# Optimization experiments

Hardware: AMD Instinct MI355X
Metric: run time of the kernel (lower is better)

Reference implementation:

```python
import jax, jax.numpy as jnp
import numpy as np

B, N, F, H, D = 2, 2048, 1024, 16, 64


def setup_inputs() -> dict:
    key = jax.random.key(0)
    ks = jax.random.split(key, 5)
    s = 0.02
    return {
        "x": jax.random.normal(ks[0], (B, N, F), jnp.float32),
        "w_qkv": (jax.random.normal(ks[1], (3 * H * D, F), jnp.float32) * s),
        "w_out": (jax.random.normal(ks[2], (F, H * D), jnp.float32) * s),
        "w_hp_pre": (jax.random.normal(ks[3], (H, H), jnp.float32) * (1.0 / H)),
        "b_hp_pre": jnp.zeros((H,), jnp.float32),
        "w_hp_post": (jax.random.normal(ks[4], (H, H), jnp.float32) * (1.0 / H)),
        "b_hp_post": jnp.zeros((H,), jnp.float32),
    }


def reference(x, w_qkv, w_out, w_hp_pre, b_hp_pre, w_hp_post, b_hp_post):
    b, n, f = x.shape
    # qkv projection; rearrange 'b n (h d qkv) -> qkv b h n d' (qkv innermost)
    proj = (x @ w_qkv.T).reshape(b, n, H, D, 3)
    q = jnp.transpose(proj[..., 0], (0, 2, 1, 3))  # b h n d
    k = jnp.transpose(proj[..., 1], (0, 2, 1, 3))
    v = jnp.transpose(proj[..., 2], (0, 2, 1, 3))
    kv = jnp.stack([k, v], axis=0)  # (2, b, h, n, d) -- returned cache

    scale = D ** -0.5
    dots = jnp.einsum('bhid,bhjd->bhij', q, k) * scale
    # pre talking-heads: 1x1 conv over head channel
    dots = jnp.einsum('gh,bhij->bgij', w_hp_pre, dots) + b_hp_pre[None, :, None, None]
    attn = jax.nn.softmax(dots, axis=-1)
    # post talking-heads
    attn = jnp.einsum('gh,bhij->bgij', w_hp_post, attn) + b_hp_post[None, :, None, None]
    out = jnp.einsum('bhij,bhjd->bhid', attn, v)
    out = jnp.transpose(out, (0, 2, 1, 3)).reshape(b, n, H * D)
    out = out @ w_out.T
    return out, kv
```

## Files before the change

### kernel.cpp

```cpp
#include <hip/hip_runtime.h>
#include <hip/hip_bf16.h>
#include <cstdint>
#include <cstddef>

#define B_ 2
#define N_ 2048
#define F_ 1024
#define H_ 16
#define D_ 64

typedef float f32x4 __attribute__((ext_vector_type(4)));
typedef short s16x8 __attribute__((ext_vector_type(8)));
typedef short s16x4 __attribute__((ext_vector_type(4)));

__device__ __forceinline__ unsigned short f2bf(float f) {
  union { __hip_bfloat16 h; unsigned short u; } c;
  c.h = __float2bfloat16(f);
  return c.u;
}

__device__ __forceinline__ void bar_lgkm() {
  asm volatile("s_waitcnt lgkmcnt(0)" ::: "memory");
  __builtin_amdgcn_s_barrier();
}

__global__ __launch_bounds__(256) void cvt_bf16(const float* __restrict__ in,
                                                unsigned short* __restrict__ out,
                                                int n8) {
  const int t = blockIdx.x * 256 + threadIdx.x;
  if (t >= n8) return;
  const float4* p = (const float4*)in + (size_t)t * 2;
  float4 a = p[0], b = p[1];
  s16x8 o;
  o[0] = f2bf(a.x); o[1] = f2bf(a.y); o[2] = f2bf(a.z); o[3] = f2bf(a.w);
  o[4] = f2bf(b.x); o[5] = f2bf(b.y); o[6] = f2bf(b.z); o[7] = f2bf(b.w);
  *((s16x8*)out + t) = o;
}

__global__ __launch_bounds__(256) void cvt_wqkv_perm(const float* __restrict__ in,
                                                     unsigned short* __restrict__ out) {
  const int t = blockIdx.x * 256 + threadIdx.x;
  const int rowp = t >> 7;
  const int kk = (t & 127) * 8;
  const int c = rowp >> 10, rem = rowp & 1023;
  const int h = rem >> 6, d = rem & 63;
  const float* p = in + (size_t)(h * 192 + d * 3 + c) * 1024 + kk;
  float4 a = *(const float4*)p, b = *(const float4*)(p + 4);
  s16x8 o;
  o[0] = f2bf(a.x); o[1] = f2bf(a.y); o[2] = f2bf(a.z); o[3] = f2bf(a.w);
  o[4] = f2bf(b.x); o[5] = f2bf(b.y); o[6] = f2bf(b.z); o[7] = f2bf(b.w);
  *((s16x8*)&out[(size_t)rowp * 1024 + kk]) = o;
}

__global__ __launch_bounds__(256) void cvt_sum4(const float* __restrict__ a,
                                                unsigned short* __restrict__ out) {
  const int t = blockIdx.x * 256 + threadIdx.x;
  const size_t stride = (size_t)B_ * N_ * 1024 / 4;
  float4 x0 = *((const float4*)a + t);
  float4 x1 = *((const float4*)a + stride + t);
  float4 x2 = *((const float4*)a + 2 * stride + t);
  float4 x3 = *((const float4*)a + 3 * stride + t);
  s16x4 o;
  o[0] = f2bf((x0.x + x1.x) + (x2.x + x3.x));
  o[1] = f2bf((x0.y + x1.y) + (x2.y + x3.y));
  o[2] = f2bf((x0.z + x1.z) + (x2.z + x3.z));
  o[3] = f2bf((x0.w + x1.w) + (x2.w + x3.w));
  *((s16x4*)out + t) = o;
}

template <int MODE>
__global__ __launch_bounds__(256) void gemm_bf16(const unsigned short* __restrict__ A,
                                                 const unsigned short* __restrict__ W,
                                                 float* __restrict__ o0,
                                                 unsigned short* __restrict__ oQ,
                                                 unsigned short* __restrict__ oK,
                                                 unsigned short* __restrict__ oVt) {
  __shared__ unsigned short As[128 * 72];
  __shared__ unsigned short Bs[128 * 72];
  const int m0 = blockIdx.y * 128, c0 = blockIdx.x * 128;
  const int tid = threadIdx.x;
  const int wave = tid >> 6, lane = tid & 63;
  const int wm = (wave & 1) * 64, wn = (wave >> 1) * 64;
  const int lm = lane & 15, lq = lane >> 4;
  f32x4 acc[4][4] = {};
  for (int k0 = 0; k0 < 1024; k0 += 64) {
#pragma unroll
    for (int it = 0; it < 4; ++it) {
      const int chunk = it * 256 + tid;
      const int row = chunk >> 3, kq = (chunk & 7) * 8;
      *(float4*)&As[row * 72 + kq] = *(const float4*)&A[(size_t)(m0 + row) * 1024 + k0 + kq];
      *(float4*)&Bs[row * 72 + kq] = *(const float4*)&W[(size_t)(c0 + row) * 1024 + k0 + kq];
    }
    __syncthreads();
#pragma unroll
    for (int ks = 0; ks < 2; ++ks) {
      s16x8 af[4], bfr[4];
#pragma unroll
      for (int i = 0; i < 4; ++i) {
        af[i] = *(const s16x8*)&As[(wm + i * 16 + lm) * 72 + ks * 32 + lq * 8];
        bfr[i] = *(const s16x8*)&Bs[(wn + i * 16 + lm) * 72 + ks * 32 + lq * 8];
      }
#pragma unroll
      for (int i = 0; i < 4; ++i)
#pragma unroll
        for (int j = 0; j < 4; ++j)
          acc[i][j] = __builtin_amdgcn_mfma_f32_16x16x32_bf16(af[i], bfr[j], acc[i][j], 0, 0, 0);
    }
    __syncthreads();
  }
  if (MODE == 1) {
#pragma unroll
    for (int i = 0; i < 4; ++i)
#pragma unroll
      for (int j = 0; j < 4; ++j)
#pragma unroll
        for (int r = 0; r < 4; ++r) {
          const int m = m0 + wm + i * 16 + lq * 4 + r;
          const int col = c0 + wn + j * 16 + lm;
          o0[(size_t)m * 1024 + col] = acc[i][j][r];
        }
  } else {
    const int cls = blockIdx.x >> 3;
    const int colbase = (blockIdx.x & 7) * 128;
    if (cls == 0) {
#pragma unroll
      for (int i = 0; i < 4; ++i)
#pragma unroll
        for (int j = 0; j < 4; ++j) {
          const int cl = colbase + wn + j * 16 + lm;
          const int h = cl >> 6, d = cl & 63;
#pragma unroll
          for (int r = 0; r < 4; ++r) {
            const int m = m0 + wm + i * 16 + lq * 4 + r;
            const int bb = m >> 11, n = m & 2047;
            oQ[(((size_t)bb * H_ + h) * N_ + n) * D_ + d] = f2bf(acc[i][j][r]);
          }
        }
    } else if (cls == 1) {
#pragma unroll
      for (int i = 0; i < 4; ++i)
#pragma unroll
        for (int j = 0; j < 4; ++j) {
          const int cl = colbase + wn + j * 16 + lm;
          const int h = cl >> 6, d = cl & 63;
#pragma unroll
          for (int r = 0; r < 4; ++r) {
            const int m = m0 + wm + i * 16 + lq * 4 + r;
            const int bb = m >> 11, n = m & 2047;
            const size_t idx = (((size_t)bb * H_ + h) * N_ + n) * D_ + d;
            o0[idx] = acc[i][j][r];
            oK[idx] = f2bf(acc[i][j][r]);
          }
        }
    } else {
#pragma unroll
      for (int i = 0; i < 4; ++i) {
        const int n0 = m0 + wm + i * 16 + lq * 4;
        const int bb = n0 >> 11, nl = n0 & 2047;
#pragma unroll
        for (int j = 0; j < 4; ++j) {
          const int cl = colbase + wn + j * 16 + lm;
          const int h = cl >> 6, d = cl & 63;
          s16x4 vp;
#pragma unroll
          for (int r = 0; r < 4; ++r) {
            const size_t idx = (((size_t)bb * H_ + h) * N_ + nl + r) * D_ + d;
            o0[(size_t)B_ * H_ * N_ * D_ + idx] = acc[i][j][r];
            vp[r] = (short)f2bf(acc[i][j][r]);
          }
          *(s16x4*)&oVt[(((size_t)bb * H_ + h) * D_ + d) * N_ + nl] = vp;
        }
      }
    }
  }
}

#define SS_J 20
#define SLOT 320
#define SS_I 644
#define SS_HALF (32 * SS_I + 16)
#define PS_J 36
#define PS_G 1156
#define PS_HALF (16 * PS_G)

__device__ __forceinline__ f32x4 mfma16(s16x8 a, s16x8 b, f32x4 c) {
  return __builtin_amdgcn_mfma_f32_16x16x32_bf16(a, b, c, 0, 0, 0);
}

__device__ __forceinline__ void load_k1(s16x8 (&kr)[2][2],
                                        const unsigned short* __restrict__ Kb,
                                        int b, int h0, int j0, int lm, int lq) {
#pragma unroll
  for (int jt = 0; jt < 2; ++jt) {
    const unsigned short* kp =
        &Kb[(((size_t)(b * H_ + h0) * N_) + j0 + jt * 16 + lm) * D_ + lq * 8];
    kr[jt][0] = *(const s16x8*)kp;
    kr[jt][1] = *(const s16x8*)(kp + 32);
  }
}

__device__ __forceinline__ void load_v1(s16x8 (&vt)[4],
                                        const unsigned short* __restrict__ Vt,
                                        int b, int h0, int j0, int lm, int lq) {
#pragma unroll
  for (int nd = 0; nd < 4; ++nd)
    vt[nd] = *(const s16x8*)&Vt[(((size_t)(b * H_ + h0) * D_) + nd * 16 + lm) * N_ + j0 + lq * 8];
}

__device__ __forceinline__ void scores_phase1(const s16x8 (&aq)[2][2],
                                              const s16x8 (&kr)[2][2],
                                              unsigned short* Sb,
                                              int lm, int lq, int h0) {
#pragma unroll
  for (int jt = 0; jt < 2; ++jt) {
    f32x4 c[2];
    __builtin_amdgcn_s_setprio(1);
#pragma unroll
    for (int mi = 0; mi < 2; ++mi) {
      f32x4 cc = {};
      cc = mfma16(aq[mi][0], kr[jt][0], cc);
      cc = mfma16(aq[mi][1], kr[jt][1], cc);
      c[mi] = cc;
    }
    __builtin_amdgcn_s_setprio(0);
#pragma unroll
    for (int mi = 0; mi < 2; ++mi)
#pragma unroll
      for (int r = 0; r < 4; ++r)
        Sb[(mi * 16 + lq * 4 + r) * SS_I + jt * SLOT + lm * SS_J + h0] = f2bf(c[mi][r]);
  }
}

__global__ __launch_bounds__(1024, 4) void attn_l(const unsigned short* __restrict__ Qb,
                                                  const unsigned short* __restrict__ Kb,
                                                  const float* __restrict__ wpre,
                                                  const float* __restrict__ bpre,
                                                  float* __restrict__ l_glob) {
  __shared__ unsigned short Ssh[SS_HALF];
  const int tid = threadIdx.x;
  const int wave = tid >> 6, lane = tid & 63;
  const int lm = lane & 15, lq = lane >> 4;
  const int b = blockIdx.z, jh = blockIdx.y;
  const int i0 = blockIdx.x * 32;
  const int j00 = jh * 512;
  const int h0 = wave;

  for (int t = tid; t < SS_HALF; t += 1024) Ssh[t] = 0;

  s16x8 aq[2][2];
#pragma unroll
  for (int mi = 0; mi < 2; ++mi)
#pragma unroll
    for (int ks = 0; ks < 2; ++ks)
      aq[mi][ks] = *(const s16x8*)&Qb[(((size_t)(b * H_ + h0) * N_) + i0 + mi * 16 + lm) * D_ + ks * 32 + lq * 8];

  s16x8 apre;
#pragma unroll
  for (int t = 0; t < 8; ++t) apre[t] = 0;
  if (lq < 2)
#pragma unroll
    for (int t = 0; t < 8; ++t) apre[t] = (short)f2bf(wpre[lm * 16 + lq * 8 + t] * 0.125f);
  float bpre_r[4];
#pragma unroll
  for (int r = 0; r < 4; ++r) bpre_r[r] = bpre[lq * 4 + r];

  float lacc[2][4] = {};

  s16x8 kr[2][2];
  load_k1(kr, Kb, b, h0, j00, lm, lq);

  for (int t = 0; t < 16; ++t) {
    bar_lgkm();
    scores_phase1(aq, kr, Ssh, lm, lq, h0);
    const int jn = j00 + (t + 1 < 16 ? (t + 1) * 32 : 480);
    load_k1(kr, Kb, b, h0, jn, lm, lq);
    bar_lgkm();
#pragma unroll
    for (int jt = 0; jt < 2; ++jt) {
      s16x4 p0[2], p1[2];
#pragma unroll
      for (int u = 0; u < 2; ++u) {
        const unsigned short* srow = &Ssh[(wave * 2 + u) * SS_I + jt * SLOT + lm * SS_J + lq * 8];
        p0[u] = *(const s16x4*)srow;
        p1[u] = *(const s16x4*)(srow + 4);
      }
#pragma unroll
      for (int u = 0; u < 2; ++u) {
        s16x8 bs;
        bs[0] = p0[u][0]; bs[1] = p0[u][1]; bs[2] = p0[u][2]; bs[3] = p0[u][3];
        bs[4] = p1[u][0]; bs[5] = p1[u][1]; bs[6] = p1[u][2]; bs[7] = p1[u][3];
        f32x4 c = {};
        c = mfma16(apre, bs, c);
#pragma unroll
        for (int r = 0; r < 4; ++r) lacc[u][r] += __expf(c[r] + bpre_r[r]);
      }
    }
  }
#pragma unroll
  for (int ig = 0; ig < 2; ++ig)
#pragma unroll
    for (int r = 0; r < 4; ++r) {
      float v = lacc[ig][r];
      v += __shfl_xor(v, 1); v += __shfl_xor(v, 2);
      v += __shfl_xor(v, 4); v += __shfl_xor(v, 8);
      if (lm == 0)
        atomicAdd(&l_glob[((size_t)b * N_ + i0 + wave * 2 + ig) * H_ + lq * 4 + r], v);
    }
}

__global__ __launch_bounds__(1024, 4) void attn_av(const unsigned short* __restrict__ Qb,
                                                   const unsigned short* __restrict__ Kb,
                                                   const unsigned short* __restrict__ Vt,
                                                   const float* __restrict__ wpre,
                                                   const float* __restrict__ bpre,
                                                   const float* __restrict__ wpost,
                                                   const float* __restrict__ bpost,
                                                   const float* __restrict__ l_glob,
                                                   float* __restrict__ Opart) {
  __shared__ unsigned short Ssh[2 * SS_HALF];
  __shared__ unsigned short Psh[2 * PS_HALF];
  __shared__ float linv[512];
  const int tid = threadIdx.x;
  const int wave = tid >> 6, lane = tid & 63;
  const int lm = lane & 15, lq = lane >> 4;
  const int b = blockIdx.z, jh = blockIdx.y;
  const int i0 = blockIdx.x * 32;
  const int j00 = jh * 512;
  const int h0 = wave;
  float* Oout = Opart + (size_t)jh * ((size_t)B_ * N_ * 1024);

  for (int t = tid; t < 2 * SS_HALF; t += 1024) Ssh[t] = 0;
  if (tid < 512)
    linv[tid] = 1.0f / l_glob[((size_t)b * N_ + i0 + (tid >> 4)) * H_ + (tid & 15)];

  s16x8 aq[2][2];
#pragma unroll
  for (int mi = 0; mi < 2; ++mi)
#pragma unroll
    for (int ks = 0; ks < 2; ++ks)
      aq[mi][ks] = *(const s16x8*)&Qb[(((size_t)(b * H_ + h0) * N_) + i0 + mi * 16 + lm) * D_ + ks * 32 + lq * 8];

  s16x8 apre, apost;
#pragma unroll
  for (int t = 0; t < 8; ++t) { apre[t] = 0; apost[t] = 0; }
  if (lq < 2)
#pragma unroll
    for (int t = 0; t < 8; ++t) {
      apre[t] = (short)f2bf(wpre[lm * 16 + lq * 8 + t] * 0.125f);
      apost[t] = (short)f2bf(wpost[lm * 16 + lq * 8 + t]);
    }
  float bpre_r[4];
#pragma unroll
  for (int r = 0; r < 4; ++r) bpre_r[r] = bpre[lq * 4 + r];
  const float bpost_lm = bpost[lm];

  const int bpA = ((((2 * lq) & 3) * 16 + lm) << 2);
  const int bpB = ((((2 * lq + 1) & 3) * 16 + lm) << 2);

  __syncthreads();

  float lifs[2][4];
#pragma unroll
  for (int u = 0; u < 2; ++u)
#pragma unroll
    for (int r = 0; r < 4; ++r)
      lifs[u][r] = linv[(wave * 2 + u) * 16 + lq * 4 + r];

  f32x4 acc[2][4] = {};

  s16x8 kr[2][2];
  load_k1(kr, Kb, b, h0, j00, lm, lq);
  s16x8 vt[4];
  load_v1(vt, Vt, b, h0, j00, lm, lq);
  scores_phase1(aq, kr, &Ssh[0], lm, lq, h0);
  load_k1(kr, Kb, b, h0, j00 + 32, lm, lq);
  bar_lgkm();

#pragma unroll 2
  for (int t = 0; t < 16; ++t) {
    unsigned short* Sc = &Ssh[(t & 1) * SS_HALF];
    unsigned short* Pc = &Psh[(t & 1) * PS_HALF];
#pragma unroll
    for (int jt = 0; jt < 2; ++jt) {
      s16x4 p0[2], p1[2];
#pragma unroll
      for (int u = 0; u < 2; ++u) {
        const unsigned short* srow = &Sc[(wave * 2 + u) * SS_I + jt * SLOT + lm * SS_J + lq * 8];
        p0[u] = *(const s16x4*)srow;
        p1[u] = *(const s16x4*)(srow + 4);
      }
      f32x4 cpre[2];
#pragma unroll
      for (int u = 0; u < 2; ++u) {
        s16x8 bs;
        bs[0] = p0[u][0]; bs[1] = p0[u][1]; bs[2] = p0[u][2]; bs[3] = p0[u][3];
        bs[4] = p1[u][0]; bs[5] = p1[u][1]; bs[6] = p1[u][2]; bs[7] = p1[u][3];
        f32x4 c = {};
        cpre[u] = mfma16(apre, bs, c);
      }
#pragma unroll
      for (int u = 0; u < 2; ++u) {
        float e0 = __expf(cpre[u][0] + bpre_r[0]) * lifs[u][0];
        float e1 = __expf(cpre[u][1] + bpre_r[1]) * lifs[u][1];
        float e2 = __expf(cpre[u][2] + bpre_r[2]) * lifs[u][2];
        float e3 = __expf(cpre[u][3] + bpre_r[3]) * lifs[u][3];
        int e01 = (int)((unsigned int)f2bf(e0) | ((unsigned int)f2bf(e1) << 16));
        int e23 = (int)((unsigned int)f2bf(e2) | ((unsigned int)f2bf(e3) << 16));
        union { int i[4]; s16x8 v; } cv;
        cv.i[0] = __builtin_amdgcn_ds_bpermute(bpA, e01);
        cv.i[1] = __builtin_amdgcn_ds_bpermute(bpA, e23);
        cv.i[2] = __builtin_amdgcn_ds_bpermute(bpB, e01);
        cv.i[3] = __builtin_amdgcn_ds_bpermute(bpB, e23);
        f32x4 c2 = {};
        c2 = mfma16(cv.v, apost, c2);
        s16x4 pv;
#pragma unroll
        for (int r = 0; r < 4; ++r) pv[r] = (short)f2bf(c2[r] + bpost_lm);
        *(s16x4*)&Pc[lm * PS_G + (wave * 2 + u) * PS_J + jt * 16 + lq * 4] = pv;
      }
    }
    if (t < 15) {
      scores_phase1(aq, kr, &Ssh[((t + 1) & 1) * SS_HALF], lm, lq, h0);
      const int jn = j00 + (t + 2 < 16 ? (t + 2) * 32 : 480);
      load_k1(kr, Kb, b, h0, jn, lm, lq);
    }
    bar_lgkm();
    s16x8 ap[2];
#pragma unroll
    for (int mi = 0; mi < 2; ++mi) {
      const unsigned short* pb = &Pc[h0 * PS_G + (mi * 16 + lm) * PS_J + lq * 8];
      s16x4 a0 = *(const s16x4*)pb;
      s16x4 a1 = *(const s16x4*)(pb + 4);
      s16x8 tt;
      tt[0] = a0[0]; tt[1] = a0[1]; tt[2] = a0[2]; tt[3] = a0[3];
      tt[4] = a1[0]; tt[5] = a1[1]; tt[6] = a1[2]; tt[7] = a1[3];
      ap[mi] = tt;
    }
    __builtin_amdgcn_s_setprio(1);
#pragma unroll
    for (int mi = 0; mi < 2; ++mi)
#pragma unroll
      for (int nd = 0; nd < 4; ++nd)
        acc[mi][nd] = mfma16(ap[mi], vt[nd], acc[mi][nd]);
    __builtin_amdgcn_s_setprio(0);
    const int jv = j00 + (t + 1 < 16 ? (t + 1) * 32 : 480);
    load_v1(vt, Vt, b, h0, jv, lm, lq);
  }
#pragma unroll
  for (int mi = 0; mi < 2; ++mi)
#pragma unroll
    for (int nd = 0; nd < 4; ++nd)
#pragma unroll
      for (int r = 0; r < 4; ++r)
        Oout[((size_t)b * N_ + i0 + mi * 16 + lq * 4 + r) * 1024 + h0 * 64 + nd * 16 + lm] = acc[mi][nd][r];
}

extern "C" void kernel_launch(void* const* d_in, const int* in_sizes, int n_in,
                              void* d_out, int out_size, void* d_ws,
                              size_t ws_size, hipStream_t stream) {
  (void)in_sizes; (void)n_in; (void)out_size; (void)ws_size;
  const float* x      = (const float*)d_in[0];
  const float* w_qkv  = (const float*)d_in[1];
  const float* w_out  = (const float*)d_in[2];
  const float* w_pre  = (const float*)d_in[3];
  const float* b_pre  = (const float*)d_in[4];
  const float* w_post = (const float*)d_in[5];
  const float* b_post = (const float*)d_in[6];

  float* out = (float*)d_out;
  float* kv  = out + (size_t)B_ * N_ * F_;

  unsigned short* xb  = (unsigned short*)d_ws;
  unsigned short* wqb = xb + (size_t)4096 * 1024;
  unsigned short* wob = wqb + (size_t)3072 * 1024;
  unsigned short* Qb  = wob + (size_t)1024 * 1024;
  unsigned short* Kb  = Qb + (size_t)B_ * H_ * N_ * D_;
  unsigned short* Vt  = Kb + (size_t)B_ * H_ * N_ * D_;
  unsigned short* O1  = Vt + (size_t)B_ * H_ * N_ * D_;
  float* l_glob = (float*)(O1 + (size_t)B_ * N_ * F_);
  float* Oh = l_glob + (size_t)B_ * N_ * H_;

  cvt_bf16<<<dim3(4096 * 1024 / 8 / 256), 256, 0, stream>>>(x, xb, 4096 * 1024 / 8);
  cvt_wqkv_perm<<<dim3(3072 * 128 / 256), 256, 0, stream>>>(w_qkv, wqb);
  cvt_bf16<<<dim3(1024 * 1024 / 8 / 256), 256, 0, stream>>>(w_out, wob, 1024 * 1024 / 8);
  hipMemsetAsync(l_glob, 0, (size_t)B_ * N_ * H_ * 4, stream);

  gemm_bf16<0><<<dim3(3072 / 128, 4096 / 128), 256, 0, stream>>>(xb, wqb, kv, Qb, Kb, Vt);

  attn_l<<<dim3(N_ / 32, 4, B_), 1024, 0, stream>>>(Qb, Kb, w_pre, b_pre, l_glob);
  attn_av<<<dim3(N_ / 32, 4, B_), 1024, 0, stream>>>(Qb, Kb, Vt, w_pre, b_pre, w_post, b_post,
                                                     l_glob, Oh);

  cvt_sum4<<<dim3(B_ * N_ * F_ / 4 / 256), 256, 0, stream>>>(Oh, O1);

  gemm_bf16<1><<<dim3(1024 / 128, 4096 / 128), 256, 0, stream>>>(O1, wob, out, nullptr, nullptr, nullptr);
}
```

Before: 383.1 us.

## Double-buffer score tiles and stagger score/softmax phases across even and odd waves

The l-pass kernel now double-buffers the score tile in shared memory, so each iteration needs one barrier instead of two. In both kernels, even waves run the premix/exp phase before the next QK^T score MMAs and odd waves do the reverse, so MFMA work and exp/LDS work from different waves overlap. The exp is rewritten as exp2 of a fused multiply-add, with the 1/l normalisation folded into the exponent bias through log2, which removes a multiply per element. Redundant tail loads are skipped and the base pointers are precomputed. The cost is more LDS in attn_l and slightly different rounding from the folded log2 normalisation.

Measured after the change: 461.9 us. 1.21x slower.

```diff
diff --git a/kernel.cpp b/kernel.cpp
--- a/kernel.cpp
+++ b/kernel.cpp
@@ -8,6 +8,7 @@
 #define F_ 1024
 #define H_ 16
 #define D_ 64
+#define LOG2E 1.44269504f
 
 typedef float f32x4 __attribute__((ext_vector_type(4)));
 typedef short s16x8 __attribute__((ext_vector_type(8)));
@@ -187,56 +188,12 @@
   return __builtin_amdgcn_mfma_f32_16x16x32_bf16(a, b, c, 0, 0, 0);
 }
 
-__device__ __forceinline__ void load_k1(s16x8 (&kr)[2][2],
-                                        const unsigned short* __restrict__ Kb,
-                                        int b, int h0, int j0, int lm, int lq) {
-#pragma unroll
-  for (int jt = 0; jt < 2; ++jt) {
-    const unsigned short* kp =
-        &Kb[(((size_t)(b * H_ + h0) * N_) + j0 + jt * 16 + lm) * D_ + lq * 8];
-    kr[jt][0] = *(const s16x8*)kp;
-    kr[jt][1] = *(const s16x8*)(kp + 32);
-  }
-}
-
-__device__ __forceinline__ void load_v1(s16x8 (&vt)[4],
-                                        const unsigned short* __restrict__ Vt,
-                                        int b, int h0, int j0, int lm, int lq) {
-#pragma unroll
-  for (int nd = 0; nd < 4; ++nd)
-    vt[nd] = *(const s16x8*)&Vt[(((size_t)(b * H_ + h0) * D_) + nd * 16 + lm) * N_ + j0 + lq * 8];
-}
-
-__device__ __forceinline__ void scores_phase1(const s16x8 (&aq)[2][2],
-                                              const s16x8 (&kr)[2][2],
-                                              unsigned short* Sb,
-                                              int lm, int lq, int h0) {
-#pragma unroll
-  for (int jt = 0; jt < 2; ++jt) {
-    f32x4 c[2];
-    __builtin_amdgcn_s_setprio(1);
-#pragma unroll
-    for (int mi = 0; mi < 2; ++mi) {
-      f32x4 cc = {};
-      cc = mfma16(aq[mi][0], kr[jt][0], cc);
-      cc = mfma16(aq[mi][1], kr[jt][1], cc);
-      c[mi] = cc;
-    }
-    __builtin_amdgcn_s_setprio(0);
-#pragma unroll
-    for (int mi = 0; mi < 2; ++mi)
-#pragma unroll
-      for (int r = 0; r < 4; ++r)
-        Sb[(mi * 16 + lq * 4 + r) * SS_I + jt * SLOT + lm * SS_J + h0] = f2bf(c[mi][r]);
-  }
-}
-
 __global__ __launch_bounds__(1024, 4) void attn_l(const unsigned short* __restrict__ Qb,
                                                   const unsigned short* __restrict__ Kb,
                                                   const float* __restrict__ wpre,
                                                   const float* __restrict__ bpre,
                                                   float* __restrict__ l_glob) {
-  __shared__ unsigned short Ssh[SS_HALF];
+  __shared__ unsigned short Ssh[2 * SS_HALF];
   const int tid = threadIdx.x;
   const int wave = tid >> 6, lane = tid & 63;
   const int lm = lane & 15, lq = lane >> 4;
@@ -245,14 +202,15 @@
   const int j00 = jh * 512;
   const int h0 = wave;
 
-  for (int t = tid; t < SS_HALF; t += 1024) Ssh[t] = 0;
-
+  for (int t = tid; t < 2 * SS_HALF; t += 1024) Ssh[t] = 0;
+
+  const unsigned short* Qw = Qb + (((size_t)(b * H_ + h0) * N_) + i0 + lm) * D_ + lq * 8;
   s16x8 aq[2][2];
 #pragma unroll
   for (int mi = 0; mi < 2; ++mi)
 #pragma unroll
     for (int ks = 0; ks < 2; ++ks)
-      aq[mi][ks] = *(const s16x8*)&Qb[(((size_t)(b * H_ + h0) * N_) + i0 + mi * 16 + lm) * D_ + ks * 32 + lq * 8];
+      aq[mi][ks] = *(const s16x8*)(Qw + mi * 16 * D_ + ks * 32);
 
   s16x8 apre;
 #pragma unroll
@@ -260,27 +218,53 @@
   if (lq < 2)
 #pragma unroll
     for (int t = 0; t < 8; ++t) apre[t] = (short)f2bf(wpre[lm * 16 + lq * 8 + t] * 0.125f);
-  float bpre_r[4];
-#pragma unroll
-  for (int r = 0; r < 4; ++r) bpre_r[r] = bpre[lq * 4 + r];
+  float bpreL[4];
+#pragma unroll
+  for (int r = 0; r < 4; ++r) bpreL[r] = bpre[lq * 4 + r] * LOG2E;
+
+  const unsigned short* Kw = Kb + (((size_t)(b * H_ + h0) * N_) + j00 + lm) * D_ + lq * 8;
 
   float lacc[2][4] = {};
-
   s16x8 kr[2][2];
-  load_k1(kr, Kb, b, h0, j00, lm, lq);
-
-  for (int t = 0; t < 16; ++t) {
-    bar_lgkm();
-    scores_phase1(aq, kr, Ssh, lm, lq, h0);
-    const int jn = j00 + (t + 1 < 16 ? (t + 1) * 32 : 480);
-    load_k1(kr, Kb, b, h0, jn, lm, lq);
-    bar_lgkm();
+
+  auto loadK = [&](int jl) {
+#pragma unroll
+    for (int jt = 0; jt < 2; ++jt) {
+      const unsigned short* kp = Kw + (size_t)(jl + jt * 16) * D_;
+      kr[jt][0] = *(const s16x8*)kp;
+      kr[jt][1] = *(const s16x8*)(kp + 32);
+    }
+  };
+  auto doScores = [&](int tt) {
+    unsigned short* Sb = &Ssh[(tt & 1) * SS_HALF];
+#pragma unroll
+    for (int jt = 0; jt < 2; ++jt) {
+      f32x4 c[2];
+      __builtin_amdgcn_s_setprio(1);
+#pragma unroll
+      for (int mi = 0; mi < 2; ++mi) {
+        f32x4 cc = {};
+        cc = mfma16(aq[mi][0], kr[jt][0], cc);
+        cc = mfma16(aq[mi][1], kr[jt][1], cc);
+        c[mi] = cc;
+      }
+      __builtin_amdgcn_s_setprio(0);
+#pragma unroll
+      for (int mi = 0; mi < 2; ++mi)
+#pragma unroll
+        for (int r = 0; r < 4; ++r)
+          Sb[(mi * 16 + lq * 4 + r) * SS_I + jt * SLOT + lm * SS_J + h0] = f2bf(c[mi][r]);
+    }
+    if (tt + 1 < 16) loadK((tt + 1) * 32);
+  };
+  auto premixSum = [&](int t) {
+    const unsigned short* Sc = &Ssh[(t & 1) * SS_HALF];
 #pragma unroll
     for (int jt = 0; jt < 2; ++jt) {
       s16x4 p0[2], p1[2];
 #pragma unroll
       for (int u = 0; u < 2; ++u) {
-        const unsigned short* srow = &Ssh[(wave * 2 + u) * SS_I + jt * SLOT + lm * SS_J + lq * 8];
+        const unsigned short* srow = &Sc[(wave * 2 + u) * SS_I + jt * SLOT + lm * SS_J + lq * 8];
         p0[u] = *(const s16x4*)srow;
         p1[u] = *(const s16x4*)(srow + 4);
       }
@@ -292,9 +276,27 @@
         f32x4 c = {};
         c = mfma16(apre, bs, c);
 #pragma unroll
-        for (int r = 0; r < 4; ++r) lacc[u][r] += __expf(c[r] + bpre_r[r]);
-      }
-    }
+        for (int r = 0; r < 4; ++r)
+          lacc[u][r] += exp2f(__fmaf_rn(c[r], LOG2E, bpreL[r]));
+      }
+    }
+  };
+
+  __syncthreads();
+
+  loadK(0);
+  doScores(0);
+  bar_lgkm();
+
+  for (int t = 0; t < 16; ++t) {
+    if ((wave & 1) == 0) {
+      premixSum(t);
+      if (t < 15) doScores(t + 1);
+    } else {
+      if (t < 15) doScores(t + 1);
+      premixSum(t);
+    }
+    bar_lgkm();
   }
 #pragma unroll
   for (int ig = 0; ig < 2; ++ig)
@@ -319,7 +321,7 @@
                                                    float* __restrict__ Opart) {
   __shared__ unsigned short Ssh[2 * SS_HALF];
   __shared__ unsigned short Psh[2 * PS_HALF];
-  __shared__ float linv[512];
+  __shared__ float linvs[512];
   const int tid = threadIdx.x;
   const int wave = tid >> 6, lane = tid & 63;
   const int lm = lane & 15, lq = lane >> 4;
@@ -331,14 +333,15 @@
 
   for (int t = tid; t < 2 * SS_HALF; t += 1024) Ssh[t] = 0;
   if (tid < 512)
-    linv[tid] = 1.0f / l_glob[((size_t)b * N_ + i0 + (tid >> 4)) * H_ + (tid & 15)];
-
+    linvs[tid] = 1.0f / l_glob[((size_t)b * N_ + i0 + (tid >> 4)) * H_ + (tid & 15)];
+
+  const unsigned short* Qw = Qb + (((size_t)(b * H_ + h0) * N_) + i0 + lm) * D_ + lq * 8;
   s16x8 aq[2][2];
 #pragma unroll
   for (int mi = 0; mi < 2; ++mi)
 #pragma unroll
     for (int ks = 0; ks < 2; ++ks)
-      aq[mi][ks] = *(const s16x8*)&Qb[(((size_t)(b * H_ + h0) * N_) + i0 + mi * 16 + lm) * D_ + ks * 32 + lq * 8];
+      aq[mi][ks] = *(const s16x8*)(Qw + mi * 16 * D_ + ks * 32);
 
   s16x8 apre, apost;
 #pragma unroll
@@ -354,31 +357,61 @@
   for (int r = 0; r < 4; ++r) bpre_r[r] = bpre[lq * 4 + r];
   const float bpost_lm = bpost[lm];
 
+  const unsigned short* Kw = Kb + (((size_t)(b * H_ + h0) * N_) + j00 + lm) * D_ + lq * 8;
+  const unsigned short* Vw = Vt + ((size_t)(b * H_ + h0) * D_ + lm) * N_ + j00 + lq * 8;
+
   const int bpA = ((((2 * lq) & 3) * 16 + lm) << 2);
   const int bpB = ((((2 * lq + 1) & 3) * 16 + lm) << 2);
 
   __syncthreads();
 
-  float lifs[2][4];
+  float bl[2][4];
 #pragma unroll
   for (int u = 0; u < 2; ++u)
 #pragma unroll
     for (int r = 0; r < 4; ++r)
-      lifs[u][r] = linv[(wave * 2 + u) * 16 + lq * 4 + r];
+      bl[u][r] = bpre_r[r] * LOG2E + log2f(linvs[(wave * 2 + u) * 16 + lq * 4 + r]);
 
   f32x4 acc[2][4] = {};
-
-  s16x8 kr[2][2];
-  load_k1(kr, Kb, b, h0, j00, lm, lq);
-  s16x8 vt[4];
-  load_v1(vt, Vt, b, h0, j00, lm, lq);
-  scores_phase1(aq, kr, &Ssh[0], lm, lq, h0);
-  load_k1(kr, Kb, b, h0, j00 + 32, lm, lq);
-  bar_lgkm();
-
-#pragma unroll 2
-  for (int t = 0; t < 16; ++t) {
-    unsigned short* Sc = &Ssh[(t & 1) * SS_HALF];
+  s16x8 kr[2][2], vt[4];
+
+  auto loadK = [&](int jl) {
+#pragma unroll
+    for (int jt = 0; jt < 2; ++jt) {
+      const unsigned short* kp = Kw + (size_t)(jl + jt * 16) * D_;
+      kr[jt][0] = *(const s16x8*)kp;
+      kr[jt][1] = *(const s16x8*)(kp + 32);
+    }
+  };
+  auto loadV = [&](int jl) {
+#pragma unroll
+    for (int nd = 0; nd < 4; ++nd)
+      vt[nd] = *(const s16x8*)(Vw + (size_t)nd * 16 * N_ + jl);
+  };
+  auto doScores = [&](int tt) {
+    unsigned short* Sb = &Ssh[(tt & 1) * SS_HALF];
+#pragma unroll
+    for (int jt = 0; jt < 2; ++jt) {
+      f32x4 c[2];
+      __builtin_amdgcn_s_setprio(1);
+#pragma unroll
+      for (int mi = 0; mi < 2; ++mi) {
+        f32x4 cc = {};
+        cc = mfma16(aq[mi][0], kr[jt][0], cc);
+        cc = mfma16(aq[mi][1], kr[jt][1], cc);
+        c[mi] = cc;
+      }
+      __builtin_amdgcn_s_setprio(0);
+#pragma unroll
+      for (int mi = 0; mi < 2; ++mi)
+#pragma unroll
+        for (int r = 0; r < 4; ++r)
+          Sb[(mi * 16 + lq * 4 + r) * SS_I + jt * SLOT + lm * SS_J + h0] = f2bf(c[mi][r]);
+    }
+    if (tt + 1 < 16) loadK((tt + 1) * 32);
+  };
+  auto phaseB = [&](int t) {
+    const unsigned short* Sc = &Ssh[(t & 1) * SS_HALF];
     unsigned short* Pc = &Psh[(t & 1) * PS_HALF];
 #pragma unroll
     for (int jt = 0; jt < 2; ++jt) {
@@ -400,10 +433,10 @@
       }
 #pragma unroll
       for (int u = 0; u < 2; ++u) {
-        float e0 = __expf(cpre[u][0] + bpre_r[0]) * lifs[u][0];
-        float e1 = __expf(cpre[u][1] + bpre_r[1]) * lifs[u][1];
-        float e2 = __expf(cpre[u][2] + bpre_r[2]) * lifs[u][2];
-        float e3 = __expf(cpre[u][3] + bpre_r[3]) * lifs[u][3];
+        float e0 = exp2f(__fmaf_rn(cpre[u][0], LOG2E, bl[u][0]));
+        float e1 = exp2f(__fmaf_rn(cpre[u][1], LOG2E, bl[u][1]));
+        float e2 = exp2f(__fmaf_rn(cpre[u][2], LOG2E, bl[u][2]));
+        float e3 = exp2f(__fmaf_rn(cpre[u][3], LOG2E, bl[u][3]));
         int e01 = (int)((unsigned int)f2bf(e0) | ((unsigned int)f2bf(e1) << 16));
         int e23 = (int)((unsigned int)f2bf(e2) | ((unsigned int)f2bf(e3) << 16));
         union { int i[4]; s16x8 v; } cv;
@@ -419,12 +452,23 @@
         *(s16x4*)&Pc[lm * PS_G + (wave * 2 + u) * PS_J + jt * 16 + lq * 4] = pv;
       }
     }
-    if (t < 15) {
-      scores_phase1(aq, kr, &Ssh[((t + 1) & 1) * SS_HALF], lm, lq, h0);
-      const int jn = j00 + (t + 2 < 16 ? (t + 2) * 32 : 480);
-      load_k1(kr, Kb, b, h0, jn, lm, lq);
+  };
+
+  loadK(0);
+  loadV(0);
+  doScores(0);
+  bar_lgkm();
+
+  for (int t = 0; t < 16; ++t) {
+    if ((wave & 1) == 0) {
+      phaseB(t);
+      if (t < 15) doScores(t + 1);
+    } else {
+      if (t < 15) doScores(t + 1);
+      phaseB(t);
     }
     bar_lgkm();
+    unsigned short* Pc = &Psh[(t & 1) * PS_HALF];
     s16x8 ap[2];
 #pragma unroll
     for (int mi = 0; mi < 2; ++mi) {
@@ -443,8 +487,7 @@
       for (int nd = 0; nd < 4; ++nd)
         acc[mi][nd] = mfma16(ap[mi], vt[nd], acc[mi][nd]);
     __builtin_amdgcn_s_setprio(0);
-    const int jv = j00 + (t + 1 < 16 ? (t + 1) * 32 : 480);
-    load_v1(vt, Vt, b, h0, jv, lm, lq);
+    if (t < 15) loadV((t + 1) * 32);
   }
 #pragma unroll
   for (int mi = 0; mi < 2; ++mi)
```

## Use direct global-to-LDS loads in GEMM and exp2 with folded normalizer

Applied to the files above, without the earlier changes.

The GEMM tile loads now use global_load_lds so data goes straight into LDS without passing through registers, and the padded 72-stride layout is dropped for an unpadded 64-stride one. In the attention kernels, exp is rewritten as exp2 of a fused multiply-add, with the bias and the log of the inverse row sum folded into one per-row offset. This removes a multiply per element. The unpadded LDS layout may cause bank conflicts on the fragment reads.

Result: slower. 405.6 us (+5.9%).

```diff
diff --git a/kernel.cpp b/kernel.cpp
--- a/kernel.cpp
+++ b/kernel.cpp
@@ -8,6 +8,7 @@
 #define F_ 1024
 #define H_ 16
 #define D_ 64
+#define LOG2E 1.44269504f
 
 typedef float f32x4 __attribute__((ext_vector_type(4)));
 typedef short s16x8 __attribute__((ext_vector_type(8)));
@@ -22,6 +23,12 @@
 __device__ __forceinline__ void bar_lgkm() {
   asm volatile("s_waitcnt lgkmcnt(0)" ::: "memory");
   __builtin_amdgcn_s_barrier();
+}
+
+__device__ __forceinline__ void gload_lds16(const void* g, void* l) {
+  __builtin_amdgcn_global_load_lds(
+      (const __attribute__((address_space(1))) void*)g,
+      (__attribute__((address_space(3))) void*)l, 16, 0, 0);
 }
 
 __global__ __launch_bounds__(256) void cvt_bf16(const float* __restrict__ in,
@@ -75,21 +82,23 @@
                                                  unsigned short* __restrict__ oQ,
                                                  unsigned short* __restrict__ oK,
                                                  unsigned short* __restrict__ oVt) {
-  __shared__ unsigned short As[128 * 72];
-  __shared__ unsigned short Bs[128 * 72];
+  __shared__ unsigned short As[128 * 64];
+  __shared__ unsigned short Bs[128 * 64];
   const int m0 = blockIdx.y * 128, c0 = blockIdx.x * 128;
   const int tid = threadIdx.x;
   const int wave = tid >> 6, lane = tid & 63;
   const int wm = (wave & 1) * 64, wn = (wave >> 1) * 64;
   const int lm = lane & 15, lq = lane >> 4;
+  const int srow = lane >> 3;
+  const int skq = (lane & 7) * 8;
   f32x4 acc[4][4] = {};
   for (int k0 = 0; k0 < 1024; k0 += 64) {
 #pragma unroll
     for (int it = 0; it < 4; ++it) {
-      const int chunk = it * 256 + tid;
-      const int row = chunk >> 3, kq = (chunk & 7) * 8;
-      *(float4*)&As[row * 72 + kq] = *(const float4*)&A[(size_t)(m0 + row) * 1024 + k0 + kq];
-      *(float4*)&Bs[row * 72 + kq] = *(const float4*)&W[(size_t)(c0 + row) * 1024 + k0 + kq];
+      const int c = wave * 4 + it;
+      const int row = c * 8 + srow;
+      gload_lds16(&A[(size_t)(m0 + row) * 1024 + k0 + skq], &As[c * 512]);
+      gload_lds16(&W[(size_t)(c0 + row) * 1024 + k0 + skq], &Bs[c * 512]);
     }
     __syncthreads();
 #pragma unroll
@@ -97,8 +106,8 @@
       s16x8 af[4], bfr[4];
 #pragma unroll
       for (int i = 0; i < 4; ++i) {
-        af[i] = *(const s16x8*)&As[(wm + i * 16 + lm) * 72 + ks * 32 + lq * 8];
-        bfr[i] = *(const s16x8*)&Bs[(wn + i * 16 + lm) * 72 + ks * 32 + lq * 8];
+        af[i] = *(const s16x8*)&As[(wm + i * 16 + lm) * 64 + ks * 32 + lq * 8];
+        bfr[i] = *(const s16x8*)&Bs[(wn + i * 16 + lm) * 64 + ks * 32 + lq * 8];
       }
 #pragma unroll
       for (int i = 0; i < 4; ++i)
@@ -260,9 +269,9 @@
   if (lq < 2)
 #pragma unroll
     for (int t = 0; t < 8; ++t) apre[t] = (short)f2bf(wpre[lm * 16 + lq * 8 + t] * 0.125f);
-  float bpre_r[4];
-#pragma unroll
-  for (int r = 0; r < 4; ++r) bpre_r[r] = bpre[lq * 4 + r];
+  float bpreL[4];
+#pragma unroll
+  for (int r = 0; r < 4; ++r) bpreL[r] = bpre[lq * 4 + r] * LOG2E;
 
   float lacc[2][4] = {};
 
@@ -292,7 +301,8 @@
         f32x4 c = {};
         c = mfma16(apre, bs, c);
 #pragma unroll
-        for (int r = 0; r < 4; ++r) lacc[u][r] += __expf(c[r] + bpre_r[r]);
+        for (int r = 0; r < 4; ++r)
+          lacc[u][r] += exp2f(__fmaf_rn(c[r], LOG2E, bpreL[r]));
       }
     }
   }
@@ -319,7 +329,7 @@
                                                    float* __restrict__ Opart) {
   __shared__ unsigned short Ssh[2 * SS_HALF];
   __shared__ unsigned short Psh[2 * PS_HALF];
-  __shared__ float linv[512];
+  __shared__ float linvs[512];
   const int tid = threadIdx.x;
   const int wave = tid >> 6, lane = tid & 63;
   const int lm = lane & 15, lq = lane >> 4;
@@ -331,7 +341,7 @@
 
   for (int t = tid; t < 2 * SS_HALF; t += 1024) Ssh[t] = 0;
   if (tid < 512)
-    linv[tid] = 1.0f / l_glob[((size_t)b * N_ + i0 + (tid >> 4)) * H_ + (tid & 15)];
+    linvs[tid] = 1.0f / l_glob[((size_t)b * N_ + i0 + (tid >> 4)) * H_ + (tid & 15)];
 
   s16x8 aq[2][2];
 #pragma unroll
@@ -359,12 +369,12 @@
 
   __syncthreads();
 
-  float lifs[2][4];
+  float bl[2][4];
 #pragma unroll
   for (int u = 0; u < 2; ++u)
 #pragma unroll
     for (int r = 0; r < 4; ++r)
-      lifs[u][r] = linv[(wave * 2 + u) * 16 + lq * 4 + r];
+      bl[u][r] = bpre_r[r] * LOG2E + log2f(linvs[(wave * 2 + u) * 16 + lq * 4 + r]);
 
   f32x4 acc[2][4] = {};
 
@@ -400,10 +410,10 @@
       }
 #pragma unroll
       for (int u = 0; u < 2; ++u) {
-        float e0 = __expf(cpre[u][0] + bpre_r[0]) * lifs[u][0];
-        float e1 = __expf(cpre[u][1] + bpre_r[1]) * lifs[u][1];
-        float e2 = __expf(cpre[u][2] + bpre_r[2]) * lifs[u][2];
-        float e3 = __expf(cpre[u][3] + bpre_r[3]) * lifs[u][3];
+        float e0 = exp2f(__fmaf_rn(cpre[u][0], LOG2E, bl[u][0]));
+        float e1 = exp2f(__fmaf_rn(cpre[u][1], LOG2E, bl[u][1]));
+        float e2 = exp2f(__fmaf_rn(cpre[u][2], LOG2E, bl[u][2]));
+        float e3 = exp2f(__fmaf_rn(cpre[u][3], LOG2E, bl[u][3]));
         int e01 = (int)((unsigned int)f2bf(e0) | ((unsigned int)f2bf(e1) << 16));
         int e23 = (int)((unsigned int)f2bf(e2) | ((unsigned int)f2bf(e3) << 16));
         union { int i[4]; s16x8 v; } cv;
```
